# Kernel optimization log

Hardware: AMD Instinct MI355X
Metric: run time of the kernel (lower is better)

The kernel has to match this reference:

```python
import jax, jax.numpy as jnp
import numpy as np

N_NODES = 50000
N_EDGES = 800000
D_IN = 128
D_OUT = 128


def _dedup_mask(src, dst, n_nodes):
    # True for exactly one representative edge per unique (src, dst) pair.
    # Equivalent to the torch unique() over cat(src_feat, dst) rows, since
    # distinct src nodes have distinct (random continuous) feature rows.
    key = src.astype(jnp.int64) * n_nodes + dst.astype(jnp.int64)
    order = jnp.argsort(key)
    ks = key[order]
    first = jnp.concatenate([jnp.array([True]), ks[1:] != ks[:-1]])
    mask = jnp.zeros(key.shape[0], dtype=bool).at[order].set(first)
    return mask


def setup_inputs() -> dict:
    key = jax.random.key(0)
    k1, k2, k3, k4, k5, k6, k7 = jax.random.split(key, 7)
    nfeats = jax.random.normal(k1, (N_NODES, D_IN), dtype=jnp.float32)
    src = jax.random.randint(k2, (N_EDGES,), 0, N_NODES, dtype=jnp.int64)
    dst = jax.random.randint(k3, (N_EDGES,), 0, N_NODES, dtype=jnp.int64)
    s1 = 1.0 / np.sqrt(D_IN)
    s2 = 1.0 / np.sqrt(D_OUT)
    W1 = jax.random.uniform(k4, (D_IN, D_OUT), jnp.float32, -s1, s1)
    b1 = jax.random.uniform(k5, (D_OUT,), jnp.float32, -s1, s1)
    W2 = jax.random.uniform(k6, (D_OUT, D_OUT), jnp.float32, -s2, s2)
    b2 = jax.random.uniform(k7, (D_OUT,), jnp.float32, -s2, s2)
    alpha = jnp.zeros((1,), dtype=jnp.float32)  # init_alpha=0, not learned
    return {"nfeats": nfeats, "src": src, "dst": dst,
            "W1": W1, "b1": b1, "W2": W2, "b2": b2, "alpha": alpha}


def reference(nfeats, src, dst, W1, b1, W2, b2, alpha):
    # message: gather src features, zero out duplicate (feat, dst) rows
    mask = _dedup_mask(src, dst, N_NODES)  # [E]
    m = nfeats[src] * mask[:, None].astype(nfeats.dtype)  # [E, D_IN]
    # sum aggregation into dst nodes
    agg = jax.ops.segment_sum(m, dst, num_segments=N_NODES)  # [N, D_IN]
    h = (1.0 + alpha[0]) * nfeats + agg
    # MLP (2 layers): Linear -> ReLU -> Linear (BatchNorms unused in source forward)
    h = jax.nn.relu(h @ W1 + b1)
    h = h @ W2 + b2
    # norm=None, act=None, dropout=0 -> identity
    return h
```

## Files before the change

kernel.cpp:

```cpp
#include <hip/hip_runtime.h>

typedef unsigned int u32;
typedef unsigned short u16;
typedef long long i64;

#define NNODES 50000
#define NEDGES 800000
#define DF 128
#define CAP 64
#define NBINS 196
#define BINCAP 5120
#define EPB 2048

typedef __bf16 bf16x8 __attribute__((ext_vector_type(8)));
typedef float f32x4 __attribute__((ext_vector_type(4)));
typedef _Float16 f16x2 __attribute__((ext_vector_type(2)));

__device__ __forceinline__ u16 f2bf(float f) {
    union { float f; u32 i; } v; v.f = f;
    u32 u = v.i;
    return (u16)((u + 0x7fffu + ((u >> 16) & 1u)) >> 16);
}
__device__ __forceinline__ u16 f2h(float f) {
    _Float16 h = (_Float16)f;
    union { _Float16 h; u16 u; } v; v.h = h;
    return v.u;
}
__device__ __forceinline__ float2 h2f2(u32 w) {
    union { u32 u; f16x2 h; } v; v.u = w;
    return make_float2((float)v.h.x, (float)v.h.y);
}

__global__ __launch_bounds__(256) void prep_kernel(const float* __restrict__ nfeats,
                                                   const float* __restrict__ W1,
                                                   const float* __restrict__ W2,
                                                   const u32* __restrict__ src_w,
                                                   u16* __restrict__ nf16,
                                                   u16* __restrict__ W1T,
                                                   u16* __restrict__ W2T,
                                                   u32* __restrict__ flag,
                                                   u32* __restrict__ cursors) {
    int bid = blockIdx.x, tid = threadIdx.x;
    if (bid < 6250) {
        int i = bid * 256 + tid;
        float4 v = ((const float4*)nfeats)[i];
        ushort4 o;
        o.x = f2h(v.x); o.y = f2h(v.y); o.z = f2h(v.z); o.w = f2h(v.w);
        ((ushort4*)nf16)[i] = o;
    } else if (bid < 6378) {
        int j = (bid - 6250) * 256 + tid;
        const float* W = (j < 16384) ? W1 : W2;
        u16* T = (j < 16384) ? W1T : W2T;
        int jj = j & 16383;
        int n = jj >> 7, k = jj & 127;
        T[jj] = f2bf(W[k * 128 + n]);
    } else {
        __shared__ int any_nz;
        for (int i = tid; i < NBINS * 16; i += 256) cursors[i] = 0u;
        if (tid == 0) any_nz = 0;
        __syncthreads();
        if (src_w[2 * tid + 1] != 0u) atomicOr(&any_nz, 1);
        __syncthreads();
        if (tid == 0) *flag = (any_nz == 0) ? 1u : 0u;
    }
}

__global__ __launch_bounds__(256) void bin_kernel(const void* __restrict__ src,
                                                  const void* __restrict__ dst,
                                                  const u32* __restrict__ flag,
                                                  u32* __restrict__ cursors,
                                                  u32* __restrict__ binbuf) {
    __shared__ u32 s_cnt[NBINS];
    __shared__ u32 s_base[NBINS];
    int t = threadIdx.x;
    for (int i = t; i < NBINS; i += 256) s_cnt[i] = 0u;
    __syncthreads();

    bool is64 = (*flag != 0u);
    int e0 = blockIdx.x * EPB + t;
    u32 pk[8];
#pragma unroll
    for (int i = 0; i < 8; ++i) {
        int e = e0 + i * 256;
        pk[i] = 0xFFFFFFFFu;
        if (e < NEDGES) {
            int s, d;
            if (is64) { s = (int)((const i64*)src)[e]; d = (int)((const i64*)dst)[e]; }
            else      { s = ((const int*)src)[e];      d = ((const int*)dst)[e]; }
            pk[i] = (u32)s | ((u32)d << 16);
            atomicAdd(&s_cnt[(u32)d >> 8], 1u);
        }
    }
    __syncthreads();
    if (t < NBINS) {
        s_base[t] = atomicAdd(&cursors[t * 16], s_cnt[t]);
        s_cnt[t] = 0u;
    }
    __syncthreads();
#pragma unroll
    for (int i = 0; i < 8; ++i) {
        if (pk[i] != 0xFFFFFFFFu) {
            u32 bin = pk[i] >> 24;
            u32 off = s_base[bin] + atomicAdd(&s_cnt[bin], 1u);
            if (off < BINCAP) binbuf[bin * BINCAP + off] = pk[i];
        }
    }
}

__global__ __launch_bounds__(256) void build_kernel(const u32* __restrict__ cursors,
                                                    const u32* __restrict__ binbuf,
                                                    u32* __restrict__ counts,
                                                    u16* __restrict__ edge16) {
    __shared__ u32 cnt[128];
    int t = threadIdx.x;
    if (t < 128) cnt[t] = 0u;
    __syncthreads();
    int b = blockIdx.x >> 1, half = blockIdx.x & 1;
    int n = (int)cursors[b * 16]; if (n > BINCAP) n = BINCAP;
    for (int i = t; i < n; i += 256) {
        u32 pk = binbuf[b * BINCAP + i];
        int dl = (int)((pk >> 16) & 0xFFu);
        if ((dl >> 7) == half) {
            u32 pos = atomicAdd(&cnt[dl & 127], 1u);
            if (pos < CAP) edge16[(((b << 8) + dl) << 6) + (int)pos] = (u16)(pk & 0xFFFFu);
        }
    }
    __syncthreads();
    if (t < 128) counts[(b << 8) + half * 128 + t] = cnt[t];
}

__global__ __launch_bounds__(256) void gather_kernel(const u16* __restrict__ nf16,
                                                     const u32* __restrict__ counts,
                                                     const u16* __restrict__ edge16,
                                                     const float* __restrict__ alpha,
                                                     float* O) {
    __shared__ __align__(16) u32 s_kept[4][CAP];
    int w = threadIdx.x >> 6, lane = threadIdx.x & 63;
    int d = blockIdx.x * 4 + w;
    int c = (int)counts[d];
    int cc = c < CAP ? c : CAP;

    float al = 1.0f + alpha[0];
    u32 rd = *(const u32*)(nf16 + (size_t)d * DF + 2 * lane);

    u32 si = 0u; bool k = false;
    if (lane < cc) { si = (u32)edge16[(d << 6) + lane]; k = true; }
    for (int j = 0; j < cc - 1; ++j) {
        u32 v = (u32)__shfl((int)si, j, 64);
        if (j < lane && v == si) k = false;
    }
    unsigned long long m = __ballot(k);
    if (k) s_kept[w][__popcll(m & ((1ull << lane) - 1ull))] = si;
    int nk = __popcll(m);
    __builtin_amdgcn_wave_barrier();

    float a0 = 0.f, a1 = 0.f;
    int i = 0;
    for (; i + 8 <= nk; i += 8) {
        int4 q0 = *(const int4*)&s_kept[w][i];
        int4 q1 = *(const int4*)&s_kept[w][i + 4];
        u32 r0 = *(const u32*)(nf16 + (size_t)(u32)q0.x * DF + 2 * lane);
        u32 r1 = *(const u32*)(nf16 + (size_t)(u32)q0.y * DF + 2 * lane);
        u32 r2 = *(const u32*)(nf16 + (size_t)(u32)q0.z * DF + 2 * lane);
        u32 r3 = *(const u32*)(nf16 + (size_t)(u32)q0.w * DF + 2 * lane);
        u32 r4 = *(const u32*)(nf16 + (size_t)(u32)q1.x * DF + 2 * lane);
        u32 r5 = *(const u32*)(nf16 + (size_t)(u32)q1.y * DF + 2 * lane);
        u32 r6 = *(const u32*)(nf16 + (size_t)(u32)q1.z * DF + 2 * lane);
        u32 r7 = *(const u32*)(nf16 + (size_t)(u32)q1.w * DF + 2 * lane);
        float2 v0 = h2f2(r0), v1 = h2f2(r1), v2 = h2f2(r2), v3 = h2f2(r3);
        float2 v4 = h2f2(r4), v5 = h2f2(r5), v6 = h2f2(r6), v7 = h2f2(r7);
        a0 += ((v0.x + v1.x) + (v2.x + v3.x)) + ((v4.x + v5.x) + (v6.x + v7.x));
        a1 += ((v0.y + v1.y) + (v2.y + v3.y)) + ((v4.y + v5.y) + (v6.y + v7.y));
    }
    for (; i + 4 <= nk; i += 4) {
        int4 q = *(const int4*)&s_kept[w][i];
        u32 r0 = *(const u32*)(nf16 + (size_t)(u32)q.x * DF + 2 * lane);
        u32 r1 = *(const u32*)(nf16 + (size_t)(u32)q.y * DF + 2 * lane);
        u32 r2 = *(const u32*)(nf16 + (size_t)(u32)q.z * DF + 2 * lane);
        u32 r3 = *(const u32*)(nf16 + (size_t)(u32)q.w * DF + 2 * lane);
        float2 v0 = h2f2(r0), v1 = h2f2(r1), v2 = h2f2(r2), v3 = h2f2(r3);
        a0 += (v0.x + v1.x) + (v2.x + v3.x);
        a1 += (v0.y + v1.y) + (v2.y + v3.y);
    }
    for (; i < nk; ++i) {
        u32 r = *(const u32*)(nf16 + (size_t)s_kept[w][i] * DF + 2 * lane);
        float2 v = h2f2(r);
        a0 += v.x; a1 += v.y;
    }

    float2 dv = h2f2(rd);
    u32 pk = (u32)f2bf(fmaf(al, dv.x, a0)) | ((u32)f2bf(fmaf(al, dv.y, a1)) << 16);
    *(u32*)((char*)O + (size_t)d * 512 + 4 * lane) = pk;
}

__global__ __launch_bounds__(256) void mlp_kernel(const u16* __restrict__ W1T,
                                                  const float* __restrict__ b1,
                                                  const u16* __restrict__ W2T,
                                                  const float* __restrict__ b2,
                                                  float* O,
                                                  int M) {
    __shared__ __align__(16) u16 sA[64][136];
    __shared__ __align__(16) u16 sW[128][136];
    __shared__ float sB[128];

    const int tid = threadIdx.x;
    const int m0 = blockIdx.x * 64;
    const int wave = tid >> 6, lane = tid & 63;
    const int lrow = lane & 15, quad = lane >> 4;
    const int warow = wave * 16;

    for (int i = tid; i < 2048; i += 256) {
        int n = i >> 4, c8 = i & 15;
        *(uint4*)((char*)(&sW[0][0]) + n * 272 + c8 * 16) = ((const uint4*)W1T)[i];
    }
    if (tid < 128) sB[tid] = b1[tid];

    for (int i = tid; i < 1024; i += 256) {
        int r = i >> 4, c8 = i & 15;
        int gr = m0 + r;
        uint4 v = make_uint4(0u, 0u, 0u, 0u);
        if (gr < M) v = *(const uint4*)((const char*)O + (size_t)gr * 512 + c8 * 16);
        *(uint4*)((char*)(&sA[0][0]) + r * 272 + c8 * 16) = v;
    }
    __syncthreads();

    {
        f32x4 acc[8];
#pragma unroll
        for (int nt = 0; nt < 8; ++nt) acc[nt] = (f32x4){0.f, 0.f, 0.f, 0.f};
#pragma unroll
        for (int kk = 0; kk < 4; ++kk) {
            bf16x8 a = *(const bf16x8*)((const char*)(&sA[0][0]) + (warow + lrow) * 272 + kk * 64 + quad * 16);
#pragma unroll
            for (int nt = 0; nt < 8; ++nt) {
                bf16x8 b = *(const bf16x8*)((const char*)(&sW[0][0]) + (nt * 16 + lrow) * 272 + kk * 64 + quad * 16);
                acc[nt] = __builtin_amdgcn_mfma_f32_16x16x32_bf16(a, b, acc[nt], 0, 0, 0);
            }
        }
#pragma unroll
        for (int nt = 0; nt < 8; ++nt) {
            int col = nt * 16 + lrow;
            float bc = sB[col];
#pragma unroll
            for (int r = 0; r < 4; ++r)
                sA[warow + quad * 4 + r][col] = f2bf(fmaxf(acc[nt][r] + bc, 0.0f));
        }
    }
    __syncthreads();

    for (int i = tid; i < 2048; i += 256) {
        int n = i >> 4, c8 = i & 15;
        *(uint4*)((char*)(&sW[0][0]) + n * 272 + c8 * 16) = ((const uint4*)W2T)[i];
    }
    if (tid < 128) sB[tid] = b2[tid];
    __syncthreads();

    {
        f32x4 acc[8];
#pragma unroll
        for (int nt = 0; nt < 8; ++nt) acc[nt] = (f32x4){0.f, 0.f, 0.f, 0.f};
#pragma unroll
        for (int kk = 0; kk < 4; ++kk) {
            bf16x8 a = *(const bf16x8*)((const char*)(&sA[0][0]) + (warow + lrow) * 272 + kk * 64 + quad * 16);
#pragma unroll
            for (int nt = 0; nt < 8; ++nt) {
                bf16x8 b = *(const bf16x8*)((const char*)(&sW[0][0]) + (nt * 16 + lrow) * 272 + kk * 64 + quad * 16);
                acc[nt] = __builtin_amdgcn_mfma_f32_16x16x32_bf16(a, b, acc[nt], 0, 0, 0);
            }
        }
#pragma unroll
        for (int nt = 0; nt < 8; ++nt) {
            int col = nt * 16 + lrow;
            float bc = sB[col];
#pragma unroll
            for (int r = 0; r < 4; ++r) {
                int grow = m0 + warow + quad * 4 + r;
                if (grow < M) O[(size_t)grow * DF + col] = acc[nt][r] + bc;
            }
        }
    }
}

extern "C" void kernel_launch(void* const* d_in, const int* in_sizes, int n_in,
                              void* d_out, int out_size, void* d_ws, size_t ws_size,
                              hipStream_t stream) {
    const float* nfeats = (const float*)d_in[0];
    const void*  src    = d_in[1];
    const void*  dst    = d_in[2];
    const float* W1     = (const float*)d_in[3];
    const float* b1     = (const float*)d_in[4];
    const float* W2     = (const float*)d_in[5];
    const float* b2     = (const float*)d_in[6];
    const float* alpha  = (const float*)d_in[7];

    char* ws = (char*)d_ws;
    u32* counts   = (u32*)ws;
    u16* edge16   = (u16*)(ws + 200704);
    u32* flag     = (u32*)(ws + 6623232);
    u16* W1T      = (u16*)(ws + 6623248);
    u16* W2T      = (u16*)(ws + 6656016);
    u16* nf16     = (u16*)(ws + 6688784);
    u32* binbuf   = (u32*)(ws + 19488784);
    u32* cursors  = (u32*)(ws + 23502864);

    prep_kernel<<<6379, 256, 0, stream>>>(nfeats, W1, W2, (const u32*)src,
                                          nf16, W1T, W2T, flag, cursors);
    bin_kernel<<<(NEDGES + EPB - 1) / EPB, 256, 0, stream>>>(src, dst, flag, cursors, binbuf);
    build_kernel<<<NBINS * 2, 256, 0, stream>>>(cursors, binbuf, counts, edge16);
    gather_kernel<<<NNODES / 4, 256, 0, stream>>>(nf16, counts, edge16, alpha, (float*)d_out);
    mlp_kernel<<<(NNODES + 63) / 64, 256, 0, stream>>>(W1T, b1, W2T, b2, (float*)d_out, NNODES);
}
```

Baseline: 174.1 us.

## Fuse binning with fp16 conversion, ballot-based dedup, padded branchless gather

The edge binning now shares a launch with the nfeats fp16 conversion and weight transposes, and a tiny init kernel zeroes the cursors and sets the dtype flag first, so binning overlaps with the conversion work. The gather kernel's duplicate detection uses readlane plus ballot instead of a per-lane shuffle loop. The kept list is padded to a multiple of eight with a zero sentinel row appended to nf16, which removes the remainder loops, and row offsets are made wave-uniform with readfirstlane. This adds an extra launch and a sentinel row, and shifts the workspace offsets.

```diff
diff --git a/kernel.cpp b/kernel.cpp
--- a/kernel.cpp
+++ b/kernel.cpp
@@ -11,9 +11,11 @@
 #define NBINS 196
 #define BINCAP 5120
 #define EPB 2048
+#define NBINB ((NEDGES + EPB - 1) / EPB)
 
 typedef __bf16 bf16x8 __attribute__((ext_vector_type(8)));
 typedef float f32x4 __attribute__((ext_vector_type(4)));
+typedef float f32x2 __attribute__((ext_vector_type(2)));
 typedef _Float16 f16x2 __attribute__((ext_vector_type(2)));
 
 __device__ __forceinline__ u16 f2bf(float f) {
@@ -26,84 +28,87 @@
     union { _Float16 h; u16 u; } v; v.h = h;
     return v.u;
 }
-__device__ __forceinline__ float2 h2f2(u32 w) {
+__device__ __forceinline__ f32x2 h2v2(u32 w) {
     union { u32 u; f16x2 h; } v; v.u = w;
-    return make_float2((float)v.h.x, (float)v.h.y);
-}
-
-__global__ __launch_bounds__(256) void prep_kernel(const float* __restrict__ nfeats,
-                                                   const float* __restrict__ W1,
-                                                   const float* __restrict__ W2,
-                                                   const u32* __restrict__ src_w,
-                                                   u16* __restrict__ nf16,
-                                                   u16* __restrict__ W1T,
-                                                   u16* __restrict__ W2T,
+    f32x2 r; r.x = (float)v.h.x; r.y = (float)v.h.y;
+    return r;
+}
+
+__global__ __launch_bounds__(256) void init_kernel(const u32* __restrict__ src_w,
                                                    u32* __restrict__ flag,
-                                                   u32* __restrict__ cursors) {
-    int bid = blockIdx.x, tid = threadIdx.x;
-    if (bid < 6250) {
-        int i = bid * 256 + tid;
+                                                   u32* __restrict__ cursors,
+                                                   u16* __restrict__ nf16) {
+    __shared__ int any_nz;
+    int tid = threadIdx.x;
+    for (int i = tid; i < NBINS * 16; i += 256) cursors[i] = 0u;
+    if (tid < 64) ((u32*)(nf16 + (size_t)NNODES * DF))[tid] = 0u;
+    if (tid == 0) any_nz = 0;
+    __syncthreads();
+    if (src_w[2 * tid + 1] != 0u) atomicOr(&any_nz, 1);
+    __syncthreads();
+    if (tid == 0) *flag = (any_nz == 0) ? 1u : 0u;
+}
+
+__global__ __launch_bounds__(256) void prepbin_kernel(const void* __restrict__ src,
+                                                      const void* __restrict__ dst,
+                                                      const u32* __restrict__ flag,
+                                                      u32* __restrict__ cursors,
+                                                      u32* __restrict__ binbuf,
+                                                      const float* __restrict__ nfeats,
+                                                      const float* __restrict__ W1,
+                                                      const float* __restrict__ W2,
+                                                      u16* __restrict__ nf16,
+                                                      u16* __restrict__ W1T,
+                                                      u16* __restrict__ W2T) {
+    __shared__ u32 s_cnt[NBINS];
+    __shared__ u32 s_base[NBINS];
+    int bid = blockIdx.x, t = threadIdx.x;
+    if (bid < NBINB) {
+        for (int i = t; i < NBINS; i += 256) s_cnt[i] = 0u;
+        __syncthreads();
+
+        bool is64 = (*flag != 0u);
+        int e0 = bid * EPB + t;
+        u32 pk[8];
+#pragma unroll
+        for (int i = 0; i < 8; ++i) {
+            int e = e0 + i * 256;
+            pk[i] = 0xFFFFFFFFu;
+            if (e < NEDGES) {
+                int s, d;
+                if (is64) { s = (int)((const i64*)src)[e]; d = (int)((const i64*)dst)[e]; }
+                else      { s = ((const int*)src)[e];      d = ((const int*)dst)[e]; }
+                pk[i] = (u32)s | ((u32)d << 16);
+                atomicAdd(&s_cnt[(u32)d >> 8], 1u);
+            }
+        }
+        __syncthreads();
+        if (t < NBINS) {
+            s_base[t] = atomicAdd(&cursors[t * 16], s_cnt[t]);
+            s_cnt[t] = 0u;
+        }
+        __syncthreads();
+#pragma unroll
+        for (int i = 0; i < 8; ++i) {
+            if (pk[i] != 0xFFFFFFFFu) {
+                u32 bin = pk[i] >> 24;
+                u32 off = s_base[bin] + atomicAdd(&s_cnt[bin], 1u);
+                if (off < BINCAP) binbuf[bin * BINCAP + off] = pk[i];
+            }
+        }
+    } else if (bid < NBINB + 6250) {
+        int i = (bid - NBINB) * 256 + t;
         float4 v = ((const float4*)nfeats)[i];
         ushort4 o;
         o.x = f2h(v.x); o.y = f2h(v.y); o.z = f2h(v.z); o.w = f2h(v.w);
         ((ushort4*)nf16)[i] = o;
-    } else if (bid < 6378) {
-        int j = (bid - 6250) * 256 + tid;
+    } else {
+        int j = (bid - NBINB - 6250) * 256 + t;
         const float* W = (j < 16384) ? W1 : W2;
         u16* T = (j < 16384) ? W1T : W2T;
         int jj = j & 16383;
         int n = jj >> 7, k = jj & 127;
         T[jj] = f2bf(W[k * 128 + n]);
-    } else {
-        __shared__ int any_nz;
-        for (int i = tid; i < NBINS * 16; i += 256) cursors[i] = 0u;
-        if (tid == 0) any_nz = 0;
-        __syncthreads();
-        if (src_w[2 * tid + 1] != 0u) atomicOr(&any_nz, 1);
-        __syncthreads();
-        if (tid == 0) *flag = (any_nz == 0) ? 1u : 0u;
-    }
-}
-
-__global__ __launch_bounds__(256) void bin_kernel(const void* __restrict__ src,
-                                                  const void* __restrict__ dst,
-                                                  const u32* __restrict__ flag,
-                                                  u32* __restrict__ cursors,
-                                                  u32* __restrict__ binbuf) {
-    __shared__ u32 s_cnt[NBINS];
-    __shared__ u32 s_base[NBINS];
-    int t = threadIdx.x;
-    for (int i = t; i < NBINS; i += 256) s_cnt[i] = 0u;
-    __syncthreads();
-
-    bool is64 = (*flag != 0u);
-    int e0 = blockIdx.x * EPB + t;
-    u32 pk[8];
-#pragma unroll
-    for (int i = 0; i < 8; ++i) {
-        int e = e0 + i * 256;
-        pk[i] = 0xFFFFFFFFu;
-        if (e < NEDGES) {
-            int s, d;
-            if (is64) { s = (int)((const i64*)src)[e]; d = (int)((const i64*)dst)[e]; }
-            else      { s = ((const int*)src)[e];      d = ((const int*)dst)[e]; }
-            pk[i] = (u32)s | ((u32)d << 16);
-            atomicAdd(&s_cnt[(u32)d >> 8], 1u);
-        }
-    }
-    __syncthreads();
-    if (t < NBINS) {
-        s_base[t] = atomicAdd(&cursors[t * 16], s_cnt[t]);
-        s_cnt[t] = 0u;
-    }
-    __syncthreads();
-#pragma unroll
-    for (int i = 0; i < 8; ++i) {
-        if (pk[i] != 0xFFFFFFFFu) {
-            u32 bin = pk[i] >> 24;
-            u32 off = s_base[bin] + atomicAdd(&s_cnt[bin], 1u);
-            if (off < BINCAP) binbuf[bin * BINCAP + off] = pk[i];
-        }
     }
 }
 
@@ -139,58 +144,58 @@
     int d = blockIdx.x * 4 + w;
     int c = (int)counts[d];
     int cc = c < CAP ? c : CAP;
+    const int lane4 = 4 * lane;
 
     float al = 1.0f + alpha[0];
-    u32 rd = *(const u32*)(nf16 + (size_t)d * DF + 2 * lane);
-
-    u32 si = 0u; bool k = false;
-    if (lane < cc) { si = (u32)edge16[(d << 6) + lane]; k = true; }
+    u32 rd = *(const u32*)((const char*)nf16 + ((size_t)d << 8) + lane4);
+
+    u32 si = 0xFFFFFFFFu;
+    if (lane < cc) si = (u32)edge16[(d << 6) + lane];
+
+    unsigned long long kill = 0ull;
     for (int j = 0; j < cc - 1; ++j) {
-        u32 v = (u32)__shfl((int)si, j, 64);
-        if (j < lane && v == si) k = false;
-    }
-    unsigned long long m = __ballot(k);
-    if (k) s_kept[w][__popcll(m & ((1ull << lane) - 1ull))] = si;
+        u32 sj = __builtin_amdgcn_readlane(si, j);
+        unsigned long long eq = __ballot(si == sj);
+        kill |= eq & ~((2ull << j) - 1ull);
+    }
+    bool keep = (lane < cc) && !((kill >> lane) & 1ull);
+    unsigned long long m = __ballot(keep);
     int nk = __popcll(m);
+    int nkp = (nk + 7) & ~7;
+    if (keep) s_kept[w][__popcll(m & ((1ull << lane) - 1ull))] = si << 8;
+    if (lane >= nk && lane < nkp) s_kept[w][lane] = ((u32)NNODES << 8);
     __builtin_amdgcn_wave_barrier();
 
-    float a0 = 0.f, a1 = 0.f;
-    int i = 0;
-    for (; i + 8 <= nk; i += 8) {
+    f32x2 acc = (f32x2){0.f, 0.f};
+    for (int i = 0; i < nkp; i += 8) {
         int4 q0 = *(const int4*)&s_kept[w][i];
         int4 q1 = *(const int4*)&s_kept[w][i + 4];
-        u32 r0 = *(const u32*)(nf16 + (size_t)(u32)q0.x * DF + 2 * lane);
-        u32 r1 = *(const u32*)(nf16 + (size_t)(u32)q0.y * DF + 2 * lane);
-        u32 r2 = *(const u32*)(nf16 + (size_t)(u32)q0.z * DF + 2 * lane);
-        u32 r3 = *(const u32*)(nf16 + (size_t)(u32)q0.w * DF + 2 * lane);
-        u32 r4 = *(const u32*)(nf16 + (size_t)(u32)q1.x * DF + 2 * lane);
-        u32 r5 = *(const u32*)(nf16 + (size_t)(u32)q1.y * DF + 2 * lane);
-        u32 r6 = *(const u32*)(nf16 + (size_t)(u32)q1.z * DF + 2 * lane);
-        u32 r7 = *(const u32*)(nf16 + (size_t)(u32)q1.w * DF + 2 * lane);
-        float2 v0 = h2f2(r0), v1 = h2f2(r1), v2 = h2f2(r2), v3 = h2f2(r3);
-        float2 v4 = h2f2(r4), v5 = h2f2(r5), v6 = h2f2(r6), v7 = h2f2(r7);
-        a0 += ((v0.x + v1.x) + (v2.x + v3.x)) + ((v4.x + v5.x) + (v6.x + v7.x));
-        a1 += ((v0.y + v1.y) + (v2.y + v3.y)) + ((v4.y + v5.y) + (v6.y + v7.y));
-    }
-    for (; i + 4 <= nk; i += 4) {
-        int4 q = *(const int4*)&s_kept[w][i];
-        u32 r0 = *(const u32*)(nf16 + (size_t)(u32)q.x * DF + 2 * lane);
-        u32 r1 = *(const u32*)(nf16 + (size_t)(u32)q.y * DF + 2 * lane);
-        u32 r2 = *(const u32*)(nf16 + (size_t)(u32)q.z * DF + 2 * lane);
-        u32 r3 = *(const u32*)(nf16 + (size_t)(u32)q.w * DF + 2 * lane);
-        float2 v0 = h2f2(r0), v1 = h2f2(r1), v2 = h2f2(r2), v3 = h2f2(r3);
-        a0 += (v0.x + v1.x) + (v2.x + v3.x);
-        a1 += (v0.y + v1.y) + (v2.y + v3.y);
-    }
-    for (; i < nk; ++i) {
-        u32 r = *(const u32*)(nf16 + (size_t)s_kept[w][i] * DF + 2 * lane);
-        float2 v = h2f2(r);
-        a0 += v.x; a1 += v.y;
-    }
-
-    float2 dv = h2f2(rd);
-    u32 pk = (u32)f2bf(fmaf(al, dv.x, a0)) | ((u32)f2bf(fmaf(al, dv.y, a1)) << 16);
-    *(u32*)((char*)O + (size_t)d * 512 + 4 * lane) = pk;
+        u32 o0 = (u32)__builtin_amdgcn_readfirstlane((int)q0.x);
+        u32 o1 = (u32)__builtin_amdgcn_readfirstlane((int)q0.y);
+        u32 o2 = (u32)__builtin_amdgcn_readfirstlane((int)q0.z);
+        u32 o3 = (u32)__builtin_amdgcn_readfirstlane((int)q0.w);
+        u32 o4 = (u32)__builtin_amdgcn_readfirstlane((int)q1.x);
+        u32 o5 = (u32)__builtin_amdgcn_readfirstlane((int)q1.y);
+        u32 o6 = (u32)__builtin_amdgcn_readfirstlane((int)q1.z);
+        u32 o7 = (u32)__builtin_amdgcn_readfirstlane((int)q1.w);
+        u32 r0 = *(const u32*)((const char*)nf16 + o0 + lane4);
+        u32 r1 = *(const u32*)((const char*)nf16 + o1 + lane4);
+        u32 r2 = *(const u32*)((const char*)nf16 + o2 + lane4);
+        u32 r3 = *(const u32*)((const char*)nf16 + o3 + lane4);
+        u32 r4 = *(const u32*)((const char*)nf16 + o4 + lane4);
+        u32 r5 = *(const u32*)((const char*)nf16 + o5 + lane4);
+        u32 r6 = *(const u32*)((const char*)nf16 + o6 + lane4);
+        u32 r7 = *(const u32*)((const char*)nf16 + o7 + lane4);
+        f32x2 t0 = h2v2(r0) + h2v2(r1);
+        f32x2 t1 = h2v2(r2) + h2v2(r3);
+        f32x2 t2 = h2v2(r4) + h2v2(r5);
+        f32x2 t3 = h2v2(r6) + h2v2(r7);
+        acc += (t0 + t1) + (t2 + t3);
+    }
+
+    f32x2 dv = h2v2(rd);
+    u32 pk = (u32)f2bf(fmaf(al, dv.x, acc.x)) | ((u32)f2bf(fmaf(al, dv.y, acc.y)) << 16);
+    *(u32*)((char*)O + (size_t)d * 512 + lane4) = pk;
 }
 
 __global__ __launch_bounds__(256) void mlp_kernel(const u16* __restrict__ W1T,
@@ -300,12 +305,12 @@
     u16* W1T      = (u16*)(ws + 6623248);
     u16* W2T      = (u16*)(ws + 6656016);
     u16* nf16     = (u16*)(ws + 6688784);
-    u32* binbuf   = (u32*)(ws + 19488784);
-    u32* cursors  = (u32*)(ws + 23502864);
-
-    prep_kernel<<<6379, 256, 0, stream>>>(nfeats, W1, W2, (const u32*)src,
-                                          nf16, W1T, W2T, flag, cursors);
-    bin_kernel<<<(NEDGES + EPB - 1) / EPB, 256, 0, stream>>>(src, dst, flag, cursors, binbuf);
+    u32* binbuf   = (u32*)(ws + 19489040);
+    u32* cursors  = (u32*)(ws + 23503120);
+
+    init_kernel<<<1, 256, 0, stream>>>((const u32*)src, flag, cursors, nf16);
+    prepbin_kernel<<<NBINB + 6250 + 128, 256, 0, stream>>>(src, dst, flag, cursors, binbuf,
+                                                           nfeats, W1, W2, nf16, W1T, W2T);
     build_kernel<<<NBINS * 2, 256, 0, stream>>>(cursors, binbuf, counts, edge16);
     gather_kernel<<<NNODES / 4, 256, 0, stream>>>(nf16, counts, edge16, alpha, (float*)d_out);
     mlp_kernel<<<(NNODES + 63) / 64, 256, 0, stream>>>(W1T, b1, W2T, b2, (float*)d_out, NNODES);
```

Result: no change. 171.1 us (-1.8%).
